# Kernel optimization log

Measured on AMD Instinct MI355X. Metric: run time of the kernel, lower is better.

Reference implementation:

```python
import jax, jax.numpy as jnp
import numpy as np
import math

B, N, P, S, C, NC = 8, 20000, 256, 32, 256, 18


def setup_inputs() -> dict:
    key = jax.random.key(0)
    ks = jax.random.split(key, 20)
    w = lambda k, shape: jax.random.normal(k, shape, jnp.float32) * 0.02
    return {
        "xyz": jax.random.normal(ks[0], (B, N, 3), jnp.float32),
        "features": jax.random.normal(ks[1], (B, C, N), jnp.float32),
        "boxes_size": jax.random.uniform(ks[2], (B, P, 3), jnp.float32, 0.2, 1.5),
        "boxes_label": jax.random.normal(ks[3], (B, P, NC), jnp.float32),
        "ts": jax.random.uniform(ks[4], (B,), jnp.float32) * 1000.0,
        "inds": jax.random.randint(ks[5], (B, P), 0, N, jnp.int32),
        # SharedMLP (259 -> 128 -> 128 -> 128), bn=False so conv1x1+bias+ReLU
        "mw0": w(ks[6], (128, C + 3)), "mb0": jnp.zeros((128,), jnp.float32),
        "mw1": w(ks[7], (128, 128)), "mb1": jnp.zeros((128,), jnp.float32),
        "mw2": w(ks[8], (128, 128)), "mb2": jnp.zeros((128,), jnp.float32),
        # label SharedMLP (18+128 -> 256 -> 256 -> 256)
        "lw0": w(ks[9], (256, NC + 128)), "lb0": jnp.zeros((256,), jnp.float32),
        "lw1": w(ks[10], (256, 256)), "lb1": jnp.zeros((256,), jnp.float32),
        "lw2": w(ks[11], (256, 256)), "lb2": jnp.zeros((256,), jnp.float32),
        # time_mlp: sinusoid(128) -> 512 -> GELU -> 512 ; block: SiLU -> 256
        "tw0": w(ks[12], (512, 128)), "tb0": jnp.zeros((512,), jnp.float32),
        "tw1": w(ks[13], (512, 512)), "tb1": jnp.zeros((512,), jnp.float32),
        "bw": w(ks[14], (256, 512)), "bb": jnp.zeros((256,), jnp.float32),
        # time_mlp_label: sinusoid(256) -> 1024 -> GELU -> 1024 ; block: SiLU -> 512
        "tlw0": w(ks[15], (1024, 256)), "tlb0": jnp.zeros((1024,), jnp.float32),
        "tlw1": w(ks[16], (1024, 1024)), "tlb1": jnp.zeros((1024,), jnp.float32),
        "blw": w(ks[17], (512, 1024)), "blb": jnp.zeros((512,), jnp.float32),
    }


def _sinusoid(t, dim):
    half = dim // 2
    freqs = jnp.exp(jnp.arange(half, dtype=jnp.float32) * (-(math.log(10000.0) / (half - 1))))
    e = t[:, None] * freqs[None, :]
    return jnp.concatenate([jnp.sin(e), jnp.cos(e)], axis=-1)


def _film(feat, ts, w0, b0, w1, b1, bw, bb, dim):
    # feat: [B, D, P]; replicates torch repeat_interleave/chunk/reshape exactly
    temb = jax.nn.gelu(_sinusoid(ts, dim) @ w0.T + b0, approximate=False) @ w1.T + b1
    ss = jax.nn.silu(temb) @ bw.T + bb          # [B, 2D]
    ss = jnp.repeat(ss, P, axis=0)              # [B*P, 2D]
    scale, shift = jnp.split(ss, 2, axis=1)
    scale = scale.reshape(-1, P)
    shift = shift.reshape(-1, P)
    f = feat.reshape(-1, P)
    return (f * (scale + 1.0) + shift).reshape(feat.shape[0], -1, P)


def reference(xyz, features, boxes_size, boxes_label, ts, inds,
              mw0, mb0, mw1, mb1, mw2, mb2,
              lw0, lb0, lw1, lb1, lw2, lb2,
              tw0, tb0, tw1, tb1, bw, bb,
              tlw0, tlb0, tlw1, tlb1, blw, blb):
    # gather proposal centers
    new_xyz = jnp.take_along_axis(xyz, inds[:, :, None], axis=1)        # [B,P,3]
    # axis-aligned box containment (the hull corners are an AABB: center +/- size/2)
    half = boxes_size * 0.5
    inside = jnp.all(jnp.abs(xyz[:, None, :, :] - new_xyz[:, :, None, :]) <= half[:, :, None, :], axis=-1)  # [B,P,N]
    # deterministic with-replacement sampling of in-box points: in-box indices first (stable sort), then cycle
    order = jnp.argsort(jnp.logical_not(inside), axis=-1)               # [B,P,N]
    count = jnp.maximum(inside.sum(axis=-1), 1)                          # [B,P]
    pos = jnp.arange(S, dtype=count.dtype)[None, None, :] % count[:, :, None]
    idx = jnp.take_along_axis(order, pos, axis=-1)                       # [B,P,S]
    b_idx = jnp.arange(B)[:, None, None]
    gxyz = xyz[b_idx, idx] - new_xyz[:, :, None, :]                      # [B,P,S,3]
    gfeat = jnp.transpose(features, (0, 2, 1))[b_idx, idx]               # [B,P,S,C]
    g = jnp.concatenate([gxyz, gfeat], axis=-1)                          # [B,P,S,3+C]
    act = lambda x, w, b: jax.nn.relu(jnp.einsum('bpsc,oc->bpso', x, w) + b)
    h = act(act(act(g, mw0, mb0), mw1, mb1), mw2, mb2)                   # [B,P,S,128]
    nf = h.max(axis=2)                                                   # [B,P,128] (max-pool over nsample)
    nf_t = jnp.transpose(nf, (0, 2, 1))                                  # [B,128,P]
    new_features = _film(nf_t, ts, tw0, tb0, tw1, tb1, bw, bb, 128)
    # label branch
    li = jnp.concatenate([boxes_label, nf], axis=-1)                     # [B,P,18+128]
    act2 = lambda x, w, b: jax.nn.relu(jnp.einsum('bpc,oc->bpo', x, w) + b)
    lf = act2(act2(act2(li, lw0, lb0), lw1, lb1), lw2, lb2)              # [B,P,256]
    lf_t = jnp.transpose(lf, (0, 2, 1))                                  # [B,256,P]
    label_feature = _film(lf_t, ts, tlw0, tlb0, tlw1, tlb1, blw, blb, 256)
    return (new_xyz, new_features, label_feature, inds)
```

## Files before the change

### kernel.cpp

```cpp
#include <hip/hip_runtime.h>
#include <math.h>

#define BB 8
#define NN 20000
#define PP 256
#define SSAMP 32
#define CC 256

typedef unsigned short u16;
typedef unsigned int u32;
typedef __attribute__((ext_vector_type(8))) short short8;
typedef __attribute__((ext_vector_type(4))) float f32x4;

__device__ __forceinline__ float b2f(u16 u) {
    union { u32 i; float f; } x; x.i = ((u32)u) << 16; return x.f;
}
__device__ __forceinline__ u16 f2b(float f) {
    union { float f; u32 i; } x; x.f = f;
    u32 i = x.i;
    i += 0x7fffu + ((i >> 16) & 1u);
    return (u16)(i >> 16);
}
__device__ __forceinline__ float rnd_bf(float f) { return b2f(f2b(f)); }
__device__ __forceinline__ float geluf(float x) {
    return 0.5f * x * (1.0f + erff(x * 0.7071067811865476f));
}
__device__ __forceinline__ float siluf(float x) {
    return x / (1.0f + expf(-x));
}
__device__ __forceinline__ f32x4 fz4() { f32x4 z = {0.f,0.f,0.f,0.f}; return z; }

__device__ __forceinline__ float ldf(const void* p, size_t i, int f32f) {
    return f32f ? ((const float*)p)[i] : b2f(((const u16*)p)[i]);
}
__device__ __forceinline__ u16 ldw(const void* p, size_t i, int f32f) {
    return f32f ? f2b(((const float*)p)[i]) : ((const u16*)p)[i];
}

__global__ void k_detect(const u16* __restrict__ xyzU, int* __restrict__ flagW) {
    int lane = threadIdx.x;
    u16 u = xyzU[(size_t)lane * 7496];
    int e = (u >> 7) & 0xFF;
    bool inR = (e >= 0x70) && (e <= 0x85);
    unsigned long long m = __ballot(inR);
    if (lane == 0) *flagW = (__popcll(m) < 48) ? 1 : 0;
}

__global__ __launch_bounds__(256) void k_repack(const int* __restrict__ flagp,
        const void* mw0, const void* mb0, const void* mw1, const void* mb1,
        const void* mw2, const void* mb2,
        const void* lw0, const void* lb0, const void* lw1, const void* lb1,
        const void* lw2, const void* lb2,
        u16* __restrict__ W0p, u16* __restrict__ W1p, u16* __restrict__ W2p,
        u16* __restrict__ L0p, u16* __restrict__ L1p, u16* __restrict__ L2p,
        float* __restrict__ biasF) {
    int f32f = *flagp;
    int i = blockIdx.x * 256 + threadIdx.x;
    if (i < 36864) {
        int o = i / 288, c = i % 288;
        u16 v = 0;
        if (c < 256) v = ldw(mw0, o * 259 + 3 + c, f32f);
        else if (c < 259) v = ldw(mw0, o * 259 + (c - 256), f32f);
        W0p[i] = v;
    } else if (i < 53248) {
        W1p[i - 36864] = ldw(mw1, i - 36864, f32f);
    } else if (i < 69632) {
        W2p[i - 53248] = ldw(mw2, i - 53248, f32f);
    } else if (i < 110592) {
        int j = i - 69632;
        int o = j / 160, c = j % 160;
        L0p[j] = (c < 146) ? ldw(lw0, o * 146 + c, f32f) : (u16)0;
    } else if (i < 176128) {
        L1p[i - 110592] = ldw(lw1, i - 110592, f32f);
    } else if (i < 241664) {
        L2p[i - 176128] = ldw(lw2, i - 176128, f32f);
    } else if (i < 242816) {
        int j = i - 241664;
        float v;
        if (j < 128) v = ldf(mb0, j, f32f);
        else if (j < 256) v = ldf(mb1, j - 128, f32f);
        else if (j < 384) v = ldf(mb2, j - 256, f32f);
        else if (j < 640) v = ldf(lb0, j - 384, f32f);
        else if (j < 896) v = ldf(lb1, j - 640, f32f);
        else v = ldf(lb2, j - 896, f32f);
        biasF[j] = v;
    }
}

__global__ __launch_bounds__(256) void k_transpose(const int* __restrict__ flagp,
                                                   const void* __restrict__ feat,
                                                   u16* __restrict__ featT, int b0) {
    __shared__ u16 tile[64][66];
    int f32f = *flagp;
    int bz = blockIdx.z, c0 = blockIdx.y * 64, n0 = blockIdx.x * 64;
    int b = b0 + bz;
    int tx = threadIdx.x, ty = threadIdx.y;
    const size_t fb = (size_t)b * CC * NN;
    for (int i = 0; i < 16; i++) {
        int cl = ty * 16 + i;
        int n = n0 + tx;
        if (n < NN) tile[cl][tx] = ldw(feat, fb + (size_t)(c0 + cl) * NN + n, f32f);
    }
    __syncthreads();
    const size_t tb = (size_t)bz * NN * CC;
    for (int i = 0; i < 16; i++) {
        int nl = ty * 16 + i;
        int n = n0 + nl;
        if (n < NN) featT[tb + (size_t)n * CC + c0 + tx] = tile[tx][nl];
    }
}

template<int ACT, int SRC>
__global__ __launch_bounds__(256) void k_lin(const int* __restrict__ flagp,
        const void* __restrict__ xin, const void* __restrict__ W,
        const void* __restrict__ bias, float* __restrict__ out, int K, int O) {
    __shared__ float xs[8 * 1024];
    int f32f = *flagp;
    int tid = threadIdx.x;
    if (SRC == 2) {
        const float* X = (const float*)xin;
        for (int i = tid; i < 8 * K; i += 256) xs[i] = X[i];
    } else {
        const int half = (SRC == 0) ? 64 : 128;
        const int dim = half * 2;
        const float cst = (SRC == 0) ? (logf(10000.f) / 63.f) : (logf(10000.f) / 127.f);
        for (int i = tid; i < 8 * dim; i += 256) {
            int b = i / dim, j = i % dim;
            float t = ldf(xin, b, f32f);
            int jj = (j < half) ? j : (j - half);
            float e = t * expf(-(float)jj * cst);
            xs[i] = (j < half) ? sinf(e) : cosf(e);
        }
    }
    __syncthreads();
    int lane = tid & 63, wv = tid >> 6;
    int r = blockIdx.x * 4 + wv;
    if (r >= O) return;
    float acc[8] = {0.f, 0.f, 0.f, 0.f, 0.f, 0.f, 0.f, 0.f};
    for (int k = lane; k < K; k += 64) {
        float wval = ldf(W, (size_t)r * K + k, f32f);
        #pragma unroll
        for (int b = 0; b < 8; b++) acc[b] += wval * xs[b * K + k];
    }
    #pragma unroll
    for (int b = 0; b < 8; b++) {
        acc[b] += __shfl_xor(acc[b], 1);
        acc[b] += __shfl_xor(acc[b], 2);
        acc[b] += __shfl_xor(acc[b], 4);
        acc[b] += __shfl_xor(acc[b], 8);
        acc[b] += __shfl_xor(acc[b], 16);
        acc[b] += __shfl_xor(acc[b], 32);
    }
    if (lane == 0) {
        float bv = ldf(bias, r, f32f);
        #pragma unroll
        for (int b = 0; b < 8; b++) {
            float v = acc[b] + bv;
            if (ACT == 1) v = geluf(v);
            else if (ACT == 2) v = siluf(v);
            out[b * O + r] = v;
        }
    }
}

__global__ __launch_bounds__(256) void k_sample(const int* __restrict__ flagp,
        const void* __restrict__ xyz,
        const void* __restrict__ bsize, const int* __restrict__ inds,
        int* __restrict__ sidx, float* __restrict__ cenW,
        float* __restrict__ outXyz, float* __restrict__ outInds) {
    __shared__ int sBuf[SSAMP];
    __shared__ int wcnt[4];
    int f32f = *flagp;
    int tid = threadIdx.x;
    int lane = tid & 63, w = tid >> 6;
    int pg = blockIdx.x;
    int b = pg >> 8;
    int ind = inds[pg];
    ind = ind < 0 ? 0 : (ind >= NN ? NN - 1 : ind);
    if (tid < SSAMP) sBuf[tid] = 0;
    size_t xb = (size_t)b * NN * 3;
    float cx = ldf(xyz, xb + (size_t)ind * 3 + 0, f32f);
    float cy = ldf(xyz, xb + (size_t)ind * 3 + 1, f32f);
    float cz = ldf(xyz, xb + (size_t)ind * 3 + 2, f32f);
    float hx = 0.5f * ldf(bsize, pg * 3 + 0, f32f);
    float hy = 0.5f * ldf(bsize, pg * 3 + 1, f32f);
    float hz = 0.5f * ldf(bsize, pg * 3 + 2, f32f);
    int cnt = 0;
    const unsigned long long lmask = (1ull << lane) - 1ull;
    for (int base = 0; base < NN; base += 1024) {
        int nb = base + w * 256 + lane;
        int nn[4];
        float px[4], py[4], pz[4];
        #pragma unroll
        for (int u = 0; u < 4; u++) {
            int n = nb + u * 64;
            nn[u] = n;
            int nc = n < NN ? n : NN - 1;
            size_t a = xb + (size_t)nc * 3;
            px[u] = ldf(xyz, a, f32f);
            py[u] = ldf(xyz, a + 1, f32f);
            pz[u] = ldf(xyz, a + 2, f32f);
        }
        bool isin[4];
        unsigned long long m[4];
        int pc[4];
        int tw = 0;
        #pragma unroll
        for (int u = 0; u < 4; u++) {
            bool in_ = (nn[u] < NN) &&
                       (fabsf(px[u] - cx) <= hx) &&
                       (fabsf(py[u] - cy) <= hy) &&
                       (fabsf(pz[u] - cz) <= hz);
            isin[u] = in_;
            m[u] = __ballot(in_);
            pc[u] = (int)__popcll(m[u]);
            tw += pc[u];
        }
        if (lane == 0) wcnt[w] = tw;
        __syncthreads();
        int w0 = wcnt[0], w1 = wcnt[1], w2 = wcnt[2], w3 = wcnt[3];
        int total = w0 + w1 + w2 + w3;
        int prior = cnt;
        if (w >= 1) prior += w0;
        if (w >= 2) prior += w1;
        if (w >= 3) prior += w2;
        #pragma unroll
        for (int u = 0; u < 4; u++) {
            int pos = prior + (int)__popcll(m[u] & lmask);
            if (isin[u] && pos < SSAMP) sBuf[pos] = nn[u];
            prior += pc[u];
        }
        __syncthreads();
        cnt += total;
        if (cnt >= SSAMP) break;
    }
    int ccap = cnt < SSAMP ? cnt : SSAMP;
    if (ccap < 1) ccap = 1;
    if (tid < SSAMP) sidx[pg * SSAMP + tid] = sBuf[tid % ccap];
    if (tid < 3) {
        float cv = tid == 0 ? cx : (tid == 1 ? cy : cz);
        outXyz[pg * 3 + tid] = cv;
        cenW[pg * 3 + tid] = cv;
    }
    if (tid == 0) outInds[pg] = rnd_bf((float)ind);
}

__global__ __launch_bounds__(256) void k_mlp1(const int* __restrict__ flagp,
        const u16* __restrict__ featT, const void* __restrict__ feat,
        int blockOff, int tier,
        const void* __restrict__ xyz, const int* __restrict__ sidx,
        const float* __restrict__ cenW, const float* __restrict__ ssW,
        const u16* __restrict__ W0p, const u16* __restrict__ W1p,
        const u16* __restrict__ W2p, const float* __restrict__ biasF,
        u16* __restrict__ nfB, float* __restrict__ outNF) {
    __shared__ u16 gA[64 * 296];
    __shared__ u16 h1s[64 * 136];
    __shared__ int nrowS[64];
    __shared__ float centS[8];
    int f32f = *flagp;
    int tid = threadIdx.x;
    int pbase = (blockIdx.x + blockOff) * 2;
    int b = pbase >> 8;
    if (tid < 64) {
        int n = sidx[pbase * SSAMP + tid];
        nrowS[tid] = n < 0 ? 0 : (n >= NN ? NN - 1 : n);
    }
    if (tid < 6) centS[tid] = cenW[pbase * 3 + tid];
    for (int e = tid; e < 64 * 32; e += 256) {
        int row = e >> 5, c2 = e & 31;
        if (c2 >= 8 && c2 < 28)
            *(u32*)&gA[row * 296 + 256 + (c2 - 8) * 2] = 0u;
    }
    __syncthreads();
    if (tier >= 1) {
        size_t rowBase = (tier == 2) ? ((size_t)b * NN) : 0;
        for (int e = tid; e < 64 * 32; e += 256) {
            int row = e >> 5, seg = e & 31;
            int n = nrowS[row];
            uint4 v = *(const uint4*)(featT + (rowBase + n) * CC + seg * 8);
            *(uint4*)&gA[row * 296 + seg * 8] = v;
        }
    } else {
        int row = tid & 63;
        int n = nrowS[row];
        const size_t fb = (size_t)b * CC * NN;
        int cbase = tid >> 6;
        for (int it = 0; it < 64; it++) {
            int cch = it * 4 + cbase;
            gA[row * 296 + cch] = ldw(feat, fb + (size_t)cch * NN + n, f32f);
        }
    }
    if (tid < 64) {
        int row = tid, q = row >> 5;
        int n = nrowS[row];
        size_t a = ((size_t)b * NN + n) * 3;
        for (int d = 0; d < 3; d++) {
            float gv = ldf(xyz, a + d, f32f) - centS[q * 3 + d];
            gA[row * 296 + 256 + d] = f2b(gv);
        }
    }
    __syncthreads();

    int lane = tid & 63, w = tid >> 6;
    int c15 = lane & 15, kq = lane >> 4;
    f32x4 acc[4][2];

    for (int mt = 0; mt < 4; mt++) for (int j = 0; j < 2; j++) acc[mt][j] = fz4();
    for (int ks = 0; ks < 9; ks++) {
        int k0 = ks * 32 + kq * 8;
        short8 af[4];
        for (int mt = 0; mt < 4; mt++)
            af[mt] = *(const short8*)&gA[(mt * 16 + c15) * 296 + k0];
        for (int j = 0; j < 2; j++) {
            int col = w * 32 + j * 16 + c15;
            short8 bf = *(const short8*)(W0p + col * 288 + k0);
            for (int mt = 0; mt < 4; mt++)
                acc[mt][j] = __builtin_amdgcn_mfma_f32_16x16x32_bf16(af[mt], bf, acc[mt][j], 0, 0, 0);
        }
    }
    for (int j = 0; j < 2; j++) {
        int col = w * 32 + j * 16 + c15;
        float bias = biasF[col];
        for (int mt = 0; mt < 4; mt++)
            for (int r = 0; r < 4; r++) {
                float v = acc[mt][j][r] + bias;
                v = v > 0.f ? v : 0.f;
                h1s[(mt * 16 + kq * 4 + r) * 136 + col] = f2b(v);
            }
    }
    __syncthreads();

    u16* h2s = gA;
    for (int mt = 0; mt < 4; mt++) for (int j = 0; j < 2; j++) acc[mt][j] = fz4();
    for (int ks = 0; ks < 4; ks++) {
        int k0 = ks * 32 + kq * 8;
        short8 af[4];
        for (int mt = 0; mt < 4; mt++)
            af[mt] = *(const short8*)&h1s[(mt * 16 + c15) * 136 + k0];
        for (int j = 0; j < 2; j++) {
            int col = w * 32 + j * 16 + c15;
            short8 bf = *(const short8*)(W1p + col * 128 + k0);
            for (int mt = 0; mt < 4; mt++)
                acc[mt][j] = __builtin_amdgcn_mfma_f32_16x16x32_bf16(af[mt], bf, acc[mt][j], 0, 0, 0);
        }
    }
    __syncthreads();
    for (int j = 0; j < 2; j++) {
        int col = w * 32 + j * 16 + c15;
        float bias = biasF[128 + col];
        for (int mt = 0; mt < 4; mt++)
            for (int r = 0; r < 4; r++) {
                float v = acc[mt][j][r] + bias;
                v = v > 0.f ? v : 0.f;
                h2s[(mt * 16 + kq * 4 + r) * 136 + col] = f2b(v);
            }
    }
    __syncthreads();

    for (int mt = 0; mt < 4; mt++) for (int j = 0; j < 2; j++) acc[mt][j] = fz4();
    for (int ks = 0; ks < 4; ks++) {
        int k0 = ks * 32 + kq * 8;
        short8 af[4];
        for (int mt = 0; mt < 4; mt++)
            af[mt] = *(const short8*)&h2s[(mt * 16 + c15) * 136 + k0];
        for (int j = 0; j < 2; j++) {
            int col = w * 32 + j * 16 + c15;
            short8 bf = *(const short8*)(W2p + col * 128 + k0);
            for (int mt = 0; mt < 4; mt++)
                acc[mt][j] = __builtin_amdgcn_mfma_f32_16x16x32_bf16(af[mt], bf, acc[mt][j], 0, 0, 0);
        }
    }
    int pA = pbase & 255, pB = (pbase + 1) & 255;
    float scA = ssW[b * 256 + (pA & 127)] + 1.f, shA = ssW[b * 256 + 128 + (pA & 127)];
    float scB = ssW[b * 256 + (pB & 127)] + 1.f, shB = ssW[b * 256 + 128 + (pB & 127)];
    for (int j = 0; j < 2; j++) {
        int col = w * 32 + j * 16 + c15;
        float bias = biasF[256 + col];
        float mA = 0.f, mB = 0.f;
        for (int mt = 0; mt < 2; mt++)
            for (int r = 0; r < 4; r++) {
                float v = acc[mt][j][r] + bias; v = v > 0.f ? v : 0.f;
                mA = fmaxf(mA, v);
            }
        for (int mt = 2; mt < 4; mt++)
            for (int r = 0; r < 4; r++) {
                float v = acc[mt][j][r] + bias; v = v > 0.f ? v : 0.f;
                mB = fmaxf(mB, v);
            }
        mA = fmaxf(mA, __shfl_xor(mA, 16)); mA = fmaxf(mA, __shfl_xor(mA, 32));
        mB = fmaxf(mB, __shfl_xor(mB, 16)); mB = fmaxf(mB, __shfl_xor(mB, 32));
        if (lane < 16) {
            nfB[(size_t)(pbase + 0) * 128 + col] = f2b(mA);
            nfB[(size_t)(pbase + 1) * 128 + col] = f2b(mB);
            outNF[((size_t)b * 128 + col) * 256 + pA] = mA * scA + shA;
            outNF[((size_t)b * 128 + col) * 256 + pB] = mB * scB + shB;
        }
    }
}

__global__ __launch_bounds__(256) void k_label(const int* __restrict__ flagp,
        const void* __restrict__ blabel,
        const u16* __restrict__ nfB, const u16* __restrict__ L0p,
        const u16* __restrict__ L1p, const u16* __restrict__ L2p,
        const float* __restrict__ biasF, const float* __restrict__ sslW,
        float* __restrict__ outLF) {
    __shared__ u16 liS[16 * 168];
    __shared__ u16 h1L[16 * 264];
    __shared__ u16 h2L[16 * 264];
    int f32f = *flagp;
    int tid = threadIdx.x;
    int pbase = blockIdx.x * 16;
    for (int e = tid; e < 16 * 160; e += 256) {
        int row = e / 160, c = e % 160;
        int pg = pbase + row;
        u16 v = 0;
        if (c < 18) v = ldw(blabel, pg * 18 + c, f32f);
        else if (c < 146) v = nfB[(size_t)pg * 128 + (c - 18)];
        liS[row * 168 + c] = v;
    }
    __syncthreads();
    int lane = tid & 63, w = tid >> 6;
    int c15 = lane & 15, kq = lane >> 4;
    f32x4 acc[4];

    for (int j = 0; j < 4; j++) acc[j] = fz4();
    for (int ks = 0; ks < 5; ks++) {
        int k0 = ks * 32 + kq * 8;
        short8 af = *(const short8*)&liS[c15 * 168 + k0];
        for (int j = 0; j < 4; j++) {
            int col = w * 64 + j * 16 + c15;
            short8 bf = *(const short8*)(L0p + col * 160 + k0);
            acc[j] = __builtin_amdgcn_mfma_f32_16x16x32_bf16(af, bf, acc[j], 0, 0, 0);
        }
    }
    for (int j = 0; j < 4; j++) {
        int col = w * 64 + j * 16 + c15;
        float bias = biasF[384 + col];
        for (int r = 0; r < 4; r++) {
            float v = acc[j][r] + bias; v = v > 0.f ? v : 0.f;
            h1L[(kq * 4 + r) * 264 + col] = f2b(v);
        }
    }
    __syncthreads();

    for (int j = 0; j < 4; j++) acc[j] = fz4();
    for (int ks = 0; ks < 8; ks++) {
        int k0 = ks * 32 + kq * 8;
        short8 af = *(const short8*)&h1L[c15 * 264 + k0];
        for (int j = 0; j < 4; j++) {
            int col = w * 64 + j * 16 + c15;
            short8 bf = *(const short8*)(L1p + col * 256 + k0);
            acc[j] = __builtin_amdgcn_mfma_f32_16x16x32_bf16(af, bf, acc[j], 0, 0, 0);
        }
    }
    for (int j = 0; j < 4; j++) {
        int col = w * 64 + j * 16 + c15;
        float bias = biasF[640 + col];
        for (int r = 0; r < 4; r++) {
            float v = acc[j][r] + bias; v = v > 0.f ? v : 0.f;
            h2L[(kq * 4 + r) * 264 + col] = f2b(v);
        }
    }
    __syncthreads();

    for (int j = 0; j < 4; j++) acc[j] = fz4();
    for (int ks = 0; ks < 8; ks++) {
        int k0 = ks * 32 + kq * 8;
        short8 af = *(const short8*)&h2L[c15 * 264 + k0];
        for (int j = 0; j < 4; j++) {
            int col = w * 64 + j * 16 + c15;
            short8 bf = *(const short8*)(L2p + col * 256 + k0);
            acc[j] = __builtin_amdgcn_mfma_f32_16x16x32_bf16(af, bf, acc[j], 0, 0, 0);
        }
    }
    for (int j = 0; j < 4; j++) {
        int col = w * 64 + j * 16 + c15;
        float bias = biasF[896 + col];
        for (int r = 0; r < 4; r++) {
            int pr = pbase + kq * 4 + r;
            int bb2 = pr >> 8, p = pr & 255;
            float v = acc[j][r] + bias; v = v > 0.f ? v : 0.f;
            float sc = sslW[bb2 * 512 + p] + 1.f;
            float sh = sslW[bb2 * 512 + 256 + p];
            outLF[((size_t)bb2 * 256 + col) * 256 + p] = v * sc + sh;
        }
    }
}

extern "C" void kernel_launch(void* const* d_in, const int* in_sizes, int n_in,
                              void* d_out, int out_size, void* d_ws, size_t ws_size,
                              hipStream_t stream) {
    const void* xyz    = d_in[0];
    const void* feat   = d_in[1];
    const void* bsize  = d_in[2];
    const void* blabel = d_in[3];
    const void* ts     = d_in[4];
    const int* inds    = (const int*)d_in[5];
    const void* mw0 = d_in[6];  const void* mb0 = d_in[7];
    const void* mw1 = d_in[8];  const void* mb1 = d_in[9];
    const void* mw2 = d_in[10]; const void* mb2 = d_in[11];
    const void* lw0 = d_in[12]; const void* lb0 = d_in[13];
    const void* lw1 = d_in[14]; const void* lb1 = d_in[15];
    const void* lw2 = d_in[16]; const void* lb2 = d_in[17];
    const void* tw0 = d_in[18]; const void* tb0 = d_in[19];
    const void* tw1 = d_in[20]; const void* tb1 = d_in[21];
    const void* bw  = d_in[22]; const void* bb  = d_in[23];
    const void* tlw0 = d_in[24]; const void* tlb0 = d_in[25];
    const void* tlw1 = d_in[26]; const void* tlb1 = d_in[27];
    const void* blw  = d_in[28]; const void* blb  = d_in[29];

    float* out = (float*)d_out;
    float* outXyz  = out;
    float* outNF   = out + 6144;
    float* outLF   = out + 268288;
    float* outInds = out + 792576;

    char* ws = (char*)d_ws;
    int*   flag  = (int*)(ws + 0);
    u16*   W0p   = (u16*)(ws + 64);
    u16*   W1p   = (u16*)(ws + 73792);
    u16*   W2p   = (u16*)(ws + 106560);
    u16*   L0p   = (u16*)(ws + 139328);
    u16*   L1p   = (u16*)(ws + 221248);
    u16*   L2p   = (u16*)(ws + 352320);
    float* biasF = (float*)(ws + 483392);
    float* ssW   = (float*)(ws + 488000);
    float* sslW  = (float*)(ws + 496192);
    float* cenW  = (float*)(ws + 512576);
    int*   sidx  = (int*)(ws + 537152);
    u16*   nfB   = (u16*)(ws + 799296);
    float* h0W   = (float*)(ws + 1323584);
    float* tembW = (float*)(ws + 1339968);
    float* g0W   = (float*)(ws + 1356352);
    float* temblW= (float*)(ws + 1389120);
    u16*   featT = (u16*)(ws + 1421888);
    const size_t NEED_A = 1421888ull + 81920000ull;
    const size_t NEED_B = 1421888ull + 10240000ull;
    int tier = (ws_size >= NEED_A) ? 2 : ((ws_size >= NEED_B) ? 1 : 0);

    k_detect<<<dim3(1), dim3(64), 0, stream>>>((const u16*)xyz, flag);
    k_repack<<<dim3(949), dim3(256), 0, stream>>>(flag, mw0, mb0, mw1, mb1, mw2, mb2,
                                                  lw0, lb0, lw1, lb1, lw2, lb2,
                                                  W0p, W1p, W2p, L0p, L1p, L2p, biasF);

    k_lin<1, 0><<<dim3(128), dim3(256), 0, stream>>>(flag, ts, tw0, tb0, h0W, 128, 512);
    k_lin<2, 2><<<dim3(128), dim3(256), 0, stream>>>(flag, h0W, tw1, tb1, tembW, 512, 512);
    k_lin<0, 2><<<dim3(64),  dim3(256), 0, stream>>>(flag, tembW, bw, bb, ssW, 512, 256);
    k_lin<1, 1><<<dim3(256), dim3(256), 0, stream>>>(flag, ts, tlw0, tlb0, g0W, 256, 1024);
    k_lin<2, 2><<<dim3(256), dim3(256), 0, stream>>>(flag, g0W, tlw1, tlb1, temblW, 1024, 1024);
    k_lin<0, 2><<<dim3(128), dim3(256), 0, stream>>>(flag, temblW, blw, blb, sslW, 1024, 512);

    k_sample<<<dim3(2048), dim3(256), 0, stream>>>(flag, xyz, bsize, inds, sidx, cenW, outXyz, outInds);

    if (tier == 2) {
        k_transpose<<<dim3(313, 4, BB), dim3(64, 4), 0, stream>>>(flag, feat, featT, 0);
        k_mlp1<<<dim3(1024), dim3(256), 0, stream>>>(flag, featT, feat, 0, 2, xyz, sidx, cenW, ssW,
                                                     W0p, W1p, W2p, biasF, nfB, outNF);
    } else if (tier == 1) {
        for (int b = 0; b < BB; b++) {
            k_transpose<<<dim3(313, 4, 1), dim3(64, 4), 0, stream>>>(flag, feat, featT, b);
            k_mlp1<<<dim3(128), dim3(256), 0, stream>>>(flag, featT, feat, b * 128, 1, xyz, sidx, cenW, ssW,
                                                        W0p, W1p, W2p, biasF, nfB, outNF);
        }
    } else {
        k_mlp1<<<dim3(1024), dim3(256), 0, stream>>>(flag, featT, feat, 0, 0, xyz, sidx, cenW, ssW,
                                                     W0p, W1p, W2p, biasF, nfB, outNF);
    }

    k_label<<<dim3(128), dim3(256), 0, stream>>>(flag, blabel, nfB, L0p, L1p, L2p, biasF, sslW, outLF);
}
```

Before: 471.5 us.

## Merge independent front-end kernels into one heterogeneous launch and inline dtype detection

```diff
diff --git a/kernel.cpp b/kernel.cpp
--- a/kernel.cpp
+++ b/kernel.cpp
@@ -37,25 +37,24 @@
     return f32f ? f2b(((const float*)p)[i]) : ((const u16*)p)[i];
 }
 
-__global__ void k_detect(const u16* __restrict__ xyzU, int* __restrict__ flagW) {
-    int lane = threadIdx.x;
-    u16 u = xyzU[(size_t)lane * 7496];
+__device__ __forceinline__ int detect_f32d(const void* xyz) {
+    int lane = threadIdx.x & 63;
+    u16 u = ((const u16*)xyz)[(size_t)lane * 7496];
     int e = (u >> 7) & 0xFF;
     bool inR = (e >= 0x70) && (e <= 0x85);
     unsigned long long m = __ballot(inR);
-    if (lane == 0) *flagW = (__popcll(m) < 48) ? 1 : 0;
-}
-
-__global__ __launch_bounds__(256) void k_repack(const int* __restrict__ flagp,
-        const void* mw0, const void* mb0, const void* mw1, const void* mb1,
-        const void* mw2, const void* mb2,
-        const void* lw0, const void* lb0, const void* lw1, const void* lb1,
-        const void* lw2, const void* lb2,
+    return (__popcll(m) < 48) ? 1 : 0;
+}
+
+__device__ __forceinline__ void repack_body(int f32f, int rb, int tid,
+        const void* mw0, const void* mw1, const void* mw2,
+        const void* lw0, const void* lw1, const void* lw2,
+        const void* mb0, const void* mb1, const void* mb2,
+        const void* lb0, const void* lb1, const void* lb2,
         u16* __restrict__ W0p, u16* __restrict__ W1p, u16* __restrict__ W2p,
         u16* __restrict__ L0p, u16* __restrict__ L1p, u16* __restrict__ L2p,
         float* __restrict__ biasF) {
-    int f32f = *flagp;
-    int i = blockIdx.x * 256 + threadIdx.x;
+    int i = rb * 256 + tid;
     if (i < 36864) {
         int o = i / 288, c = i % 288;
         u16 v = 0;
@@ -87,14 +86,12 @@
     }
 }
 
-__global__ __launch_bounds__(256) void k_transpose(const int* __restrict__ flagp,
-                                                   const void* __restrict__ feat,
-                                                   u16* __restrict__ featT, int b0) {
-    __shared__ u16 tile[64][66];
-    int f32f = *flagp;
-    int bz = blockIdx.z, c0 = blockIdx.y * 64, n0 = blockIdx.x * 64;
+__device__ __forceinline__ void transpose_body(int f32f, const void* __restrict__ feat,
+        u16* __restrict__ featT, int n0i, int c0i, int bz, int b0, int tid,
+        u16 (*tile)[66]) {
+    int c0 = c0i * 64, n0 = n0i * 64;
     int b = b0 + bz;
-    int tx = threadIdx.x, ty = threadIdx.y;
+    int tx = tid & 63, ty = tid >> 6;
     const size_t fb = (size_t)b * CC * NN;
     for (int i = 0; i < 16; i++) {
         int cl = ty * 16 + i;
@@ -111,12 +108,9 @@
 }
 
 template<int ACT, int SRC>
-__global__ __launch_bounds__(256) void k_lin(const int* __restrict__ flagp,
-        const void* __restrict__ xin, const void* __restrict__ W,
-        const void* __restrict__ bias, float* __restrict__ out, int K, int O) {
-    __shared__ float xs[8 * 1024];
-    int f32f = *flagp;
-    int tid = threadIdx.x;
+__device__ __forceinline__ void lin_body(int f32f, const void* __restrict__ xin,
+        const void* __restrict__ W, const void* __restrict__ bias,
+        float* __restrict__ out, int K, int O, int rb, int tid, float* xs) {
     if (SRC == 2) {
         const float* X = (const float*)xin;
         for (int i = tid; i < 8 * K; i += 256) xs[i] = X[i];
@@ -134,7 +128,7 @@
     }
     __syncthreads();
     int lane = tid & 63, wv = tid >> 6;
-    int r = blockIdx.x * 4 + wv;
+    int r = rb * 4 + wv;
     if (r >= O) return;
     float acc[8] = {0.f, 0.f, 0.f, 0.f, 0.f, 0.f, 0.f, 0.f};
     for (int k = lane; k < K; k += 64) {
@@ -163,17 +157,12 @@
     }
 }
 
-__global__ __launch_bounds__(256) void k_sample(const int* __restrict__ flagp,
-        const void* __restrict__ xyz,
+__device__ __forceinline__ void sample_body(int f32f, const void* __restrict__ xyz,
         const void* __restrict__ bsize, const int* __restrict__ inds,
         int* __restrict__ sidx, float* __restrict__ cenW,
-        float* __restrict__ outXyz, float* __restrict__ outInds) {
-    __shared__ int sBuf[SSAMP];
-    __shared__ int wcnt[4];
-    int f32f = *flagp;
-    int tid = threadIdx.x;
+        float* __restrict__ outXyz, float* __restrict__ outInds,
+        int pg, int tid, int* sBuf, int* wcnt) {
     int lane = tid & 63, w = tid >> 6;
-    int pg = blockIdx.x;
     int b = pg >> 8;
     int ind = inds[pg];
     ind = ind < 0 ? 0 : (ind >= NN ? NN - 1 : ind);
@@ -185,9 +174,9 @@
     float hx = 0.5f * ldf(bsize, pg * 3 + 0, f32f);
     float hy = 0.5f * ldf(bsize, pg * 3 + 1, f32f);
     float hz = 0.5f * ldf(bsize, pg * 3 + 2, f32f);
-    int cnt = 0;
+    int cnt = 0, par = 0;
     const unsigned long long lmask = (1ull << lane) - 1ull;
-    for (int base = 0; base < NN; base += 1024) {
+    for (int base = 0; base < NN; base += 1024, par ^= 4) {
         int nb = base + w * 256 + lane;
         int nn[4];
         float px[4], py[4], pz[4];
@@ -216,9 +205,9 @@
             pc[u] = (int)__popcll(m[u]);
             tw += pc[u];
         }
-        if (lane == 0) wcnt[w] = tw;
+        if (lane == 0) wcnt[par + w] = tw;
         __syncthreads();
-        int w0 = wcnt[0], w1 = wcnt[1], w2 = wcnt[2], w3 = wcnt[3];
+        int w0 = wcnt[par + 0], w1 = wcnt[par + 1], w2 = wcnt[par + 2], w3 = wcnt[par + 3];
         int total = w0 + w1 + w2 + w3;
         int prior = cnt;
         if (w >= 1) prior += w0;
@@ -230,10 +219,10 @@
             if (isin[u] && pos < SSAMP) sBuf[pos] = nn[u];
             prior += pc[u];
         }
-        __syncthreads();
         cnt += total;
         if (cnt >= SSAMP) break;
     }
+    __syncthreads();
     int ccap = cnt < SSAMP ? cnt : SSAMP;
     if (ccap < 1) ccap = 1;
     if (tid < SSAMP) sidx[pg * SSAMP + tid] = sBuf[tid % ccap];
@@ -245,7 +234,80 @@
     if (tid == 0) outInds[pg] = rnd_bf((float)ind);
 }
 
-__global__ __launch_bounds__(256) void k_mlp1(const int* __restrict__ flagp,
+__global__ __launch_bounds__(256) void k_front(
+        const void* __restrict__ xyz, const void* __restrict__ feat,
+        const void* __restrict__ bsize, const int* __restrict__ inds,
+        const void* __restrict__ ts,
+        const void* mw0, const void* mw1, const void* mw2,
+        const void* lw0, const void* lw1, const void* lw2,
+        const void* mb0, const void* mb1, const void* mb2,
+        const void* lb0, const void* lb1, const void* lb2,
+        const void* tw0, const void* tb0,
+        const void* tlw0, const void* tlb0,
+        u16* __restrict__ featT, int nTrans,
+        int* __restrict__ sidx, float* __restrict__ cenW,
+        float* __restrict__ outXyz, float* __restrict__ outInds,
+        u16* __restrict__ W0p, u16* __restrict__ W1p, u16* __restrict__ W2p,
+        u16* __restrict__ L0p, u16* __restrict__ L1p, u16* __restrict__ L2p,
+        float* __restrict__ biasF, float* __restrict__ h0W, float* __restrict__ g0W) {
+    __shared__ __align__(16) char smem[8448];
+    int tid = threadIdx.x;
+    int f32f = detect_f32d(xyz);
+    unsigned bx = blockIdx.x;
+    unsigned s1 = 2048u + (unsigned)nTrans;
+    unsigned s2 = s1 + 949u;
+    unsigned s3 = s2 + 128u;
+    if (bx < 2048u) {
+        sample_body(f32f, xyz, bsize, inds, sidx, cenW, outXyz, outInds,
+                    (int)bx, tid, (int*)smem, (int*)(smem + 128));
+    } else if (bx < s1) {
+        int t = (int)(bx - 2048u);
+        transpose_body(f32f, feat, featT, t % 313, (t / 313) & 3, t / 1252, 0, tid,
+                       (u16(*)[66])smem);
+    } else if (bx < s2) {
+        repack_body(f32f, (int)(bx - s1), tid, mw0, mw1, mw2, lw0, lw1, lw2,
+                    mb0, mb1, mb2, lb0, lb1, lb2, W0p, W1p, W2p, L0p, L1p, L2p, biasF);
+    } else if (bx < s3) {
+        lin_body<1, 0>(f32f, ts, tw0, tb0, h0W, 128, 512, (int)(bx - s2), tid, (float*)smem);
+    } else {
+        lin_body<1, 1>(f32f, ts, tlw0, tlb0, g0W, 256, 1024, (int)(bx - s3), tid, (float*)smem);
+    }
+}
+
+__global__ __launch_bounds__(256) void k_mid2(const void* __restrict__ xyz,
+        const void* tw1, const void* tb1, const void* tlw1, const void* tlb1,
+        const float* __restrict__ h0W, const float* __restrict__ g0W,
+        float* __restrict__ tembW, float* __restrict__ temblW) {
+    __shared__ float xs[8 * 1024];
+    int tid = threadIdx.x;
+    int f32f = detect_f32d(xyz);
+    unsigned bx = blockIdx.x;
+    if (bx < 128u) lin_body<2, 2>(f32f, h0W, tw1, tb1, tembW, 512, 512, (int)bx, tid, xs);
+    else lin_body<2, 2>(f32f, g0W, tlw1, tlb1, temblW, 1024, 1024, (int)(bx - 128u), tid, xs);
+}
+
+__global__ __launch_bounds__(256) void k_mid3(const void* __restrict__ xyz,
+        const void* bw, const void* bb, const void* blw, const void* blb,
+        const float* __restrict__ tembW, const float* __restrict__ temblW,
+        float* __restrict__ ssW, float* __restrict__ sslW) {
+    __shared__ float xs[8 * 1024];
+    int tid = threadIdx.x;
+    int f32f = detect_f32d(xyz);
+    unsigned bx = blockIdx.x;
+    if (bx < 64u) lin_body<0, 2>(f32f, tembW, bw, bb, ssW, 512, 256, (int)bx, tid, xs);
+    else lin_body<0, 2>(f32f, temblW, blw, blb, sslW, 1024, 512, (int)(bx - 64u), tid, xs);
+}
+
+__global__ __launch_bounds__(256) void k_transpose(const void* __restrict__ xyz,
+                                                   const void* __restrict__ feat,
+                                                   u16* __restrict__ featT, int b0) {
+    __shared__ u16 tile[64][66];
+    int f32f = detect_f32d(xyz);
+    transpose_body(f32f, feat, featT, blockIdx.x, blockIdx.y, blockIdx.z, b0,
+                   threadIdx.x, tile);
+}
+
+__global__ __launch_bounds__(256) void k_mlp1(
         const u16* __restrict__ featT, const void* __restrict__ feat,
         int blockOff, int tier,
         const void* __restrict__ xyz, const int* __restrict__ sidx,
@@ -257,7 +319,7 @@
     __shared__ u16 h1s[64 * 136];
     __shared__ int nrowS[64];
     __shared__ float centS[8];
-    int f32f = *flagp;
+    int f32f = detect_f32d(xyz);
     int tid = threadIdx.x;
     int pbase = (blockIdx.x + blockOff) * 2;
     int b = pbase >> 8;
@@ -398,7 +460,7 @@
     }
 }
 
-__global__ __launch_bounds__(256) void k_label(const int* __restrict__ flagp,
+__global__ __launch_bounds__(256) void k_label(const void* __restrict__ xyz,
         const void* __restrict__ blabel,
         const u16* __restrict__ nfB, const u16* __restrict__ L0p,
         const u16* __restrict__ L1p, const u16* __restrict__ L2p,
@@ -407,7 +469,7 @@
     __shared__ u16 liS[16 * 168];
     __shared__ u16 h1L[16 * 264];
     __shared__ u16 h2L[16 * 264];
-    int f32f = *flagp;
+    int f32f = detect_f32d(xyz);
     int tid = threadIdx.x;
     int pbase = blockIdx.x * 16;
     for (int e = tid; e < 16 * 160; e += 256) {
@@ -516,7 +578,6 @@
     float* outInds = out + 792576;
 
     char* ws = (char*)d_ws;
-    int*   flag  = (int*)(ws + 0);
     u16*   W0p   = (u16*)(ws + 64);
     u16*   W1p   = (u16*)(ws + 73792);
     u16*   W2p   = (u16*)(ws + 106560);
@@ -538,34 +599,34 @@
     const size_t NEED_B = 1421888ull + 10240000ull;
     int tier = (ws_size >= NEED_A) ? 2 : ((ws_size >= NEED_B) ? 1 : 0);
 
-    k_detect<<<dim3(1), dim3(64), 0, stream>>>((const u16*)xyz, flag);
-    k_repack<<<dim3(949), dim3(256), 0, stream>>>(flag, mw0, mb0, mw1, mb1, mw2, mb2,
-                                                  lw0, lb0, lw1, lb1, lw2, lb2,
-                                                  W0p, W1p, W2p, L0p, L1p, L2p, biasF);
-
-    k_lin<1, 0><<<dim3(128), dim3(256), 0, stream>>>(flag, ts, tw0, tb0, h0W, 128, 512);
-    k_lin<2, 2><<<dim3(128), dim3(256), 0, stream>>>(flag, h0W, tw1, tb1, tembW, 512, 512);
-    k_lin<0, 2><<<dim3(64),  dim3(256), 0, stream>>>(flag, tembW, bw, bb, ssW, 512, 256);
-    k_lin<1, 1><<<dim3(256), dim3(256), 0, stream>>>(flag, ts, tlw0, tlb0, g0W, 256, 1024);
-    k_lin<2, 2><<<dim3(256), dim3(256), 0, stream>>>(flag, g0W, tlw1, tlb1, temblW, 1024, 1024);
-    k_lin<0, 2><<<dim3(128), dim3(256), 0, stream>>>(flag, temblW, blw, blb, sslW, 1024, 512);
-
-    k_sample<<<dim3(2048), dim3(256), 0, stream>>>(flag, xyz, bsize, inds, sidx, cenW, outXyz, outInds);
+    int nTrans = (tier == 2) ? 10016 : 0;
+    unsigned gFront = 2048u + (unsigned)nTrans + 949u + 128u + 256u;
+    k_front<<<dim3(gFront), dim3(256), 0, stream>>>(
+        xyz, feat, bsize, inds, ts,
+        mw0, mw1, mw2, lw0, lw1, lw2,
+        mb0, mb1, mb2, lb0, lb1, lb2,
+        tw0, tb0, tlw0, tlb0,
+        featT, nTrans, sidx, cenW, outXyz, outInds,
+        W0p, W1p, W2p, L0p, L1p, L2p, biasF, h0W, g0W);
+
+    k_mid2<<<dim3(384), dim3(256), 0, stream>>>(xyz, tw1, tb1, tlw1, tlb1,
+                                                h0W, g0W, tembW, temblW);
+    k_mid3<<<dim3(192), dim3(256), 0, stream>>>(xyz, bw, bb, blw, blb,
+                                                tembW, temblW, ssW, sslW);
 
     if (tier == 2) {
-        k_transpose<<<dim3(313, 4, BB), dim3(64, 4), 0, stream>>>(flag, feat, featT, 0);
-        k_mlp1<<<dim3(1024), dim3(256), 0, stream>>>(flag, featT, feat, 0, 2, xyz, sidx, cenW, ssW,
+        k_mlp1<<<dim3(1024), dim3(256), 0, stream>>>(featT, feat, 0, 2, xyz, sidx, cenW, ssW,
                                                      W0p, W1p, W2p, biasF, nfB, outNF);
     } else if (tier == 1) {
         for (int b = 0; b < BB; b++) {
-            k_transpose<<<dim3(313, 4, 1), dim3(64, 4), 0, stream>>>(flag, feat, featT, b);
-            k_mlp1<<<dim3(128), dim3(256), 0, stream>>>(flag, featT, feat, b * 128, 1, xyz, sidx, cenW, ssW,
+            k_transpose<<<dim3(313, 4, 1), dim3(256), 0, stream>>>(xyz, feat, featT, b);
+            k_mlp1<<<dim3(128), dim3(256), 0, stream>>>(featT, feat, b * 128, 1, xyz, sidx, cenW, ssW,
                                                         W0p, W1p, W2p, biasF, nfB, outNF);
         }
     } else {
-        k_mlp1<<<dim3(1024), dim3(256), 0, stream>>>(flag, featT, feat, 0, 0, xyz, sidx, cenW, ssW,
+        k_mlp1<<<dim3(1024), dim3(256), 0, stream>>>(featT, feat, 0, 0, xyz, sidx, cenW, ssW,
                                                      W0p, W1p, W2p, biasF, nfB, outNF);
     }
 
-    k_label<<<dim3(128), dim3(256), 0, stream>>>(flag, blabel, nfB, L0p, L1p, L2p, biasF, sslW, outLF);
-}
+    k_label<<<dim3(128), dim3(256), 0, stream>>>(xyz, blabel, nfB, L0p, L1p, L2p, biasF, sslW, outLF);
+}
```

New measurement: 427.5 us. -9.3%, faster.
